# Optimization experiments

Hardware: AMD Instinct MI355X
Metric: run time of the kernel (lower is better)

The kernel has to match this reference:

```python
import jax, jax.numpy as jnp
import numpy as np
from jax import lax

EPS = 1e-12  # torch F.normalize eps


def _unfold3(x):
    # x: [B,C,H,W] -> [B, C*9, H*W]; matches torch F.unfold(k=3, stride=1, pad=1)
    # channel ordering (c, kh, kw), i.e. index = c*9 + kh*3 + kw
    B, C, H, W = x.shape
    xp = jnp.pad(x, ((0, 0), (0, 0), (1, 1), (1, 1)))
    pats = jnp.stack([xp[:, :, i:i + H, j:j + W] for i in range(3) for j in range(3)], axis=2)  # [B,C,9,H,W]
    return pats.reshape(B, C * 9, H * W)


def _fold3(u, H, W):
    # inverse of _unfold3 with overlap-add (torch F.fold, k=3, stride=1, pad=1)
    B, CK, L = u.shape
    C = CK // 9
    u = u.reshape(B, C, 3, 3, H, W)
    canvas = jnp.zeros((B, C, H + 2, W + 2), u.dtype)
    for i in range(3):
        for j in range(3):
            canvas = canvas.at[:, :, i:i + H, j:j + W].add(u[:, :, i, j])
    return canvas[:, :, 1:H + 1, 1:W + 1]


def setup_inputs() -> dict:
    key = jax.random.key(0)
    k1, k2, k3, k4, k5, k6 = jax.random.split(key, 6)
    B, C, H, W = 4, 64, 64, 64
    lr = jax.random.normal(k1, (B, C, H, W), dtype=jnp.float32)
    ref = jax.random.normal(k2, (B, C, H, W), dtype=jnp.float32)
    # fusion: Conv2d(2C, C, 1) then depthwise Conv2d(C, C, 3, groups=C), both with bias
    w1 = jax.random.normal(k3, (C, 2 * C, 1, 1), dtype=jnp.float32) * 0.05
    b1 = jax.random.normal(k4, (C,), dtype=jnp.float32) * 0.05
    wd = jax.random.normal(k5, (C, 1, 3, 3), dtype=jnp.float32) * 0.05
    bd = jax.random.normal(k6, (C,), dtype=jnp.float32) * 0.05
    return {"lr": lr, "ref": ref, "w1": w1, "b1": b1, "wd": wd, "bd": bd}


def reference(lr, ref, w1, b1, wd, bd):
    B, C, H, W = ref.shape
    ref_u = _unfold3(ref)          # [B, 9C, L]
    lr_u = _unfold3(lr)            # [B, 9C, L]
    ref_t = ref_u.transpose(0, 2, 1)  # [B, L, 9C]
    ref_n = ref_t / jnp.maximum(jnp.linalg.norm(ref_t, axis=2, keepdims=True), EPS)
    lr_n = lr_u / jnp.maximum(jnp.linalg.norm(lr_u, axis=1, keepdims=True), EPS)
    R = jnp.einsum('bld,bdm->blm', ref_n, lr_n)  # [B, L, L] cosine correlation
    arg = jnp.argmax(R, axis=1)                  # [B, L] best ref patch per lr position
    T_u = jnp.take_along_axis(ref_u, jnp.broadcast_to(arg[:, None, :], ref_u.shape), axis=2)
    T = _fold3(T_u, H, W)                        # [B, C, H, W]
    x = jnp.concatenate([lr, T], axis=1)         # [B, 2C, H, W]
    dn = ('NCHW', 'OIHW', 'NCHW')
    y = lax.conv_general_dilated(x, w1, (1, 1), 'VALID', dimension_numbers=dn) + b1[None, :, None, None]
    y = lax.conv_general_dilated(y, wd, (1, 1), ((1, 1), (1, 1)), dimension_numbers=dn,
                                 feature_group_count=C) + bd[None, :, None, None]
    return jax.nn.relu(y)
```

## Files before the change

### kernel.cpp

```cpp
#include <hip/hip_runtime.h>
#include <cstdint>
#include <cstddef>


#define BATCH 4
#define CCH 64
#define LPIX 4096
typedef unsigned long long u64;

__device__ __forceinline__ u64 packKey(float v, int idx) {
    unsigned int bits = __float_as_uint(v);
    unsigned int m = (bits & 0x80000000u) ? ~bits : (bits | 0x80000000u);
    return ((u64)m << 32) | (unsigned int)(~(unsigned int)idx);
}

__global__ __launch_bounds__(256) void prep_kernel(const float* __restrict__ ref,
                                                   float* __restrict__ refT,
                                                   float* __restrict__ ssq) {
    __shared__ float s[64 * 65];
    __shared__ float part[256];
    int pt = blockIdx.x, b = blockIdx.y, tid = threadIdx.x;
    const float* rb = ref + ((size_t)b * CCH) * LPIX + pt * 64;
    for (int k = 0; k < 16; ++k) {
        int n = tid + 256 * k;
        int c = n >> 6, p = n & 63;
        s[c * 65 + p] = rb[(size_t)c * LPIX + p];
    }
    __syncthreads();
    {
        int p = tid & 63, g = tid >> 6;
        float acc = 0.f;
        for (int c = g * 16; c < g * 16 + 16; ++c) { float v = s[c * 65 + p]; acc += v * v; }
        part[g * 64 + p] = acc;
    }
    __syncthreads();
    if (tid < 64) {
        float v = part[tid] + part[64 + tid] + part[128 + tid] + part[192 + tid];
        ssq[b * LPIX + pt * 64 + tid] = v;
    }
    float* tb = refT + ((size_t)b * LPIX + pt * 64) * 64;
    for (int k = 0; k < 16; ++k) {
        int n = tid + 256 * k;
        int p = n >> 6, c = n & 63;
        tb[n] = s[c * 65 + p];
    }
}

__global__ __launch_bounds__(256) void invnorm_kernel(const float* __restrict__ ssq,
                                                      float* __restrict__ inv) {
    int t = blockIdx.x * 256 + threadIdx.x;
    int b = t >> 12, p = t & 4095;
    int y = p >> 6, x = p & 63;
    const float* sb = ssq + b * LPIX;
    float n2 = 0.f;
    for (int i = -1; i <= 1; ++i)
        for (int j = -1; j <= 1; ++j) {
            int yy = y + i, xx = x + j;
            if (yy >= 0 && yy < 64 && xx >= 0 && xx < 64) n2 += sb[yy * 64 + xx];
        }
    inv[t] = 1.0f / fmaxf(sqrtf(n2), 1e-12f);
}

__global__ __launch_bounds__(256, 2) void gemmE_kernel(const float* __restrict__ ref,
                                                       const float* __restrict__ lr,
                                                       float* __restrict__ E) {
    __shared__ __align__(16) float As[2 * 4096];
    __shared__ __align__(16) float Bs[2 * 4096];
    int bx = blockIdx.x, by = blockIdx.y, b = blockIdx.z, tid = threadIdx.x;
    const float* Ab = ref + (size_t)b * CCH * LPIX;
    const float* Bb = lr + (size_t)b * CCH * LPIX;
#pragma unroll
    for (int kk = 0; kk < 8; ++kk) {
        int n = tid + 256 * kk;
        int h = n >> 10, c = (n >> 4) & 63, q = n & 15;
        *(float4*)&As[h * 4096 + c * 64 + 4 * q] =
            *(const float4*)&Ab[(size_t)c * LPIX + (2 * by + h) * 64 + 4 * q];
        *(float4*)&Bs[h * 4096 + c * 64 + 4 * q] =
            *(const float4*)&Bb[(size_t)c * LPIX + (2 * bx + h) * 64 + 4 * q];
    }
    __syncthreads();
    int w = tid >> 6, lane = tid & 63, rg = lane >> 3, cg = lane & 7;
    const float* Ap = As + (w >> 1) * 4096 + rg * 8;
    const float* Bp = Bs + (w & 1) * 4096 + cg * 8;
    float acc[8][8] = {};
#pragma unroll 4
    for (int k = 0; k < 64; ++k) {
        float4 a0 = *(const float4*)(Ap + k * 64);
        float4 a1 = *(const float4*)(Ap + k * 64 + 4);
        float4 b0 = *(const float4*)(Bp + k * 64);
        float4 b1 = *(const float4*)(Bp + k * 64 + 4);
        float av[8] = {a0.x, a0.y, a0.z, a0.w, a1.x, a1.y, a1.z, a1.w};
        float bv[8] = {b0.x, b0.y, b0.z, b0.w, b1.x, b1.y, b1.z, b1.w};
#pragma unroll
        for (int i = 0; i < 8; ++i)
#pragma unroll
            for (int j = 0; j < 8; ++j) acc[i][j] = fmaf(av[i], bv[j], acc[i][j]);
    }
    float up[7], lf[7], dn[8], rt[8], um, dpc;
#pragma unroll
    for (int t = 0; t < 7; ++t) up[t] = __shfl(acc[7][t], lane - 8, 64);
    um = __shfl(acc[7][7], lane - 9, 64);
#pragma unroll
    for (int t = 0; t < 7; ++t) lf[t] = __shfl(acc[t][7], lane - 1, 64);
#pragma unroll
    for (int t = 1; t < 8; ++t) dn[t] = __shfl(acc[0][t], lane + 8, 64);
    dpc = __shfl(acc[0][0], lane + 9, 64);
#pragma unroll
    for (int t = 1; t < 8; ++t) rt[t] = __shfl(acc[t][0], lane + 1, 64);

    int r1 = 2 * by + (w >> 1), r2 = 2 * bx + (w & 1);
    float* Et = E + ((size_t)b << 24) + ((size_t)((r1 << 6) + r2) << 12) + (rg * 8) * 64 + cg * 8;
    bool rgt = rg > 0, rlt = rg < 7, cgt = cg > 0, clt = cg < 7;
#pragma unroll
    for (int i = 0; i < 8; ++i) {
        float e[8];
#pragma unroll
        for (int j = 0; j < 8; ++j) {
            float dm, dpv;
            if (i >= 1) dm = (j >= 1) ? acc[i - 1][j - 1] : (cgt ? lf[i - 1] : 0.f);
            else        dm = rgt ? ((j >= 1) ? up[j - 1] : (cgt ? um : 0.f)) : 0.f;
            if (i <= 6) dpv = (j <= 6) ? acc[i + 1][j + 1] : (clt ? rt[i + 1] : 0.f);
            else        dpv = rlt ? ((j <= 6) ? dn[j + 1] : (clt ? dpc : 0.f)) : 0.f;
            e[j] = dm + acc[i][j] + dpv;
        }
        *(float4*)(Et + i * 64)     = make_float4(e[0], e[1], e[2], e[3]);
        *(float4*)(Et + i * 64 + 4) = make_float4(e[4], e[5], e[6], e[7]);
    }
}

__global__ __launch_bounds__(256) void band_kernel(const float* __restrict__ E,
                                                   const float* __restrict__ inv,
                                                   u64* __restrict__ packed) {
    __shared__ u64 red[16 * 65];
    int b = blockIdx.z;
    int k = (int)blockIdx.y - 63;
    int t_lo = k < 0 ? -k : 0;
    int t_hi = 64 - (k > 0 ? k : 0);
    int y0 = t_lo + (int)blockIdx.x * 16;
    if (y0 >= t_hi) return;
    int y1 = y0 + 16 < t_hi ? y0 + 16 : t_hi;
    const float* Ebase = E + ((size_t)b << 24);
    const float* invb = inv + b * LPIX;
    u64* pkb = packed + (size_t)b * LPIX;
    int tid = threadIdx.x;
    int c4 = tid & 15, s = tid >> 4;

    float4 Ea[4], Eb[4], Ec[4];
    auto LOADT = [&](float4* T, int t) {
        if (t >= t_lo && t < t_hi) {
            const float4* tp = (const float4*)(Ebase + ((size_t)(((t + k) << 6) + t) << 12));
#pragma unroll
            for (int i = 0; i < 4; ++i) T[i] = tp[tid + 256 * i];
        } else {
#pragma unroll
            for (int i = 0; i < 4; ++i) T[i] = make_float4(0.f, 0.f, 0.f, 0.f);
        }
    };
    LOADT(Ea, y0 - 1); LOADT(Eb, y0); LOADT(Ec, y0 + 1);

    for (int y = y0; y < y1; ++y) {
        int yprow = (y + k) << 6;
        u64 kc0 = 0, kc1 = 0, kc2 = 0, kc3 = 0;
#pragma unroll
        for (int i = 0; i < 4; ++i) {
            int xr = s + 16 * i;
            float iv = invb[yprow + xr];
            int idx = yprow + xr;
            float vx = (Ea[i].x + Eb[i].x + Ec[i].x) * iv;
            float vy = (Ea[i].y + Eb[i].y + Ec[i].y) * iv;
            float vz = (Ea[i].z + Eb[i].z + Ec[i].z) * iv;
            float vw = (Ea[i].w + Eb[i].w + Ec[i].w) * iv;
            u64 t0 = packKey(vx, idx); kc0 = kc0 > t0 ? kc0 : t0;
            u64 t1 = packKey(vy, idx); kc1 = kc1 > t1 ? kc1 : t1;
            u64 t2 = packKey(vz, idx); kc2 = kc2 > t2 ? kc2 : t2;
            u64 t3 = packKey(vw, idx); kc3 = kc3 > t3 ? kc3 : t3;
        }
        red[s * 65 + 4 * c4 + 0] = kc0;
        red[s * 65 + 4 * c4 + 1] = kc1;
        red[s * 65 + 4 * c4 + 2] = kc2;
        red[s * 65 + 4 * c4 + 3] = kc3;
        __syncthreads();
        if (tid < 64) {
            u64 m = red[tid];
#pragma unroll
            for (int ss = 1; ss < 16; ++ss) {
                u64 v = red[ss * 65 + tid];
                m = m > v ? m : v;
            }
            atomicMax(&pkb[(y << 6) + tid], m);
        }
        __syncthreads();
        if (y + 1 < y1) {
            float4 En[4];
            LOADT(En, y + 2);
#pragma unroll
            for (int i = 0; i < 4; ++i) { Ea[i] = Eb[i]; Eb[i] = Ec[i]; Ec[i] = En[i]; }
        }
    }
}

__global__ __launch_bounds__(256) void gather_kernel(const u64* __restrict__ packed,
                                                     const float* __restrict__ refT,
                                                     float* __restrict__ Tt) {
    int b = blockIdx.y;
    int wave = threadIdx.x >> 6, lane = threadIdx.x & 63;
    int p = blockIdx.x * 4 + wave;
    int py = p >> 6, px = p & 63;
    const u64* pk = packed + (size_t)b * LPIX;
    const float* rT = refT + (size_t)b * LPIX * 64;
    float acc = 0.f;
#pragma unroll
    for (int i = 0; i < 3; ++i)
#pragma unroll
        for (int j = 0; j < 3; ++j) {
            int qy = py + 1 - i, qx = px + 1 - j;
            if ((unsigned)qy >= 64u || (unsigned)qx >= 64u) continue;
            int aidx = (int)(~(unsigned int)pk[qy * 64 + qx]);
            int ry = (aidx >> 6) + i - 1, rx = (aidx & 63) + j - 1;
            if ((unsigned)ry >= 64u || (unsigned)rx >= 64u) continue;
            acc += rT[(size_t)(ry * 64 + rx) * 64 + lane];
        }
    Tt[((size_t)b * LPIX + p) * 64 + lane] = acc;
}

#define XST 36
__global__ __launch_bounds__(256) void conv1_kernel(const float* __restrict__ lr,
                                                    const float* __restrict__ Tt,
                                                    const float* __restrict__ w1,
                                                    const float* __restrict__ b1,
                                                    float* __restrict__ z) {
    __shared__ __align__(16) float xs[128 * XST];
    __shared__ __align__(16) float wsm[64 * 128];
    int pt = blockIdx.x, b = blockIdx.y, tid = threadIdx.x;
    for (int k = 0; k < 8; ++k) {
        int n = tid + 256 * k;
        *(float4*)&wsm[4 * n] = *(const float4*)&w1[4 * n];
    }
    const float* lrb = lr + (size_t)b * CCH * LPIX + pt * 32;
    for (int k = 0; k < 2; ++k) {
        int n = tid + 256 * k;
        int c = n >> 3, q = n & 7;
        *(float4*)&xs[c * XST + 4 * q] = *(const float4*)&lrb[(size_t)c * LPIX + 4 * q];
    }
    const float* Tb = Tt + ((size_t)b * LPIX + pt * 32) * 64;
    for (int k = 0; k < 2; ++k) {
        int n = tid + 256 * k;
        int p = n >> 4, cq = n & 15;
        float4 v = *(const float4*)&Tb[p * 64 + 4 * cq];
        xs[(64 + 4 * cq + 0) * XST + p] = v.x;
        xs[(64 + 4 * cq + 1) * XST + p] = v.y;
        xs[(64 + 4 * cq + 2) * XST + p] = v.z;
        xs[(64 + 4 * cq + 3) * XST + p] = v.w;
    }
    __syncthreads();
    int p = tid & 31, g = tid >> 5;
    float acc[8];
#pragma unroll
    for (int t = 0; t < 8; ++t) acc[t] = b1[g * 8 + t];
    for (int c = 0; c < 128; ++c) {
        float xv = xs[c * XST + p];
#pragma unroll
        for (int t = 0; t < 8; ++t) acc[t] = fmaf(wsm[(g * 8 + t) * 128 + c], xv, acc[t]);
    }
    float* zb = z + (size_t)b * CCH * LPIX + pt * 32;
#pragma unroll
    for (int t = 0; t < 8; ++t) zb[(size_t)(g * 8 + t) * LPIX + p] = acc[t];
}

__global__ __launch_bounds__(256) void dw_kernel(const float* __restrict__ z,
                                                 const float* __restrict__ wd,
                                                 const float* __restrict__ bd,
                                                 float* __restrict__ out) {
    __shared__ __align__(16) float zs[4096];
    int c = blockIdx.x, b = blockIdx.y, tid = threadIdx.x;
    const float* zb = z + ((size_t)b * CCH + c) * LPIX;
    for (int k = 0; k < 4; ++k) {
        int n = tid + 256 * k;
        *(float4*)&zs[4 * n] = *(const float4*)&zb[4 * n];
    }
    __syncthreads();
    float w[9];
#pragma unroll
    for (int t = 0; t < 9; ++t) w[t] = wd[c * 9 + t];
    float bias = bd[c];
    float* ob = out + ((size_t)b * CCH + c) * LPIX;
    for (int s = 0; s < 16; ++s) {
        int p = tid + 256 * s;
        int y = p >> 6, x = p & 63;
        float acc = bias;
#pragma unroll
        for (int i = 0; i < 3; ++i) {
            int yy = y + i - 1;
            if ((unsigned)yy >= 64u) continue;
#pragma unroll
            for (int j = 0; j < 3; ++j) {
                int xx = x + j - 1;
                if ((unsigned)xx >= 64u) continue;
                acc = fmaf(zs[yy * 64 + xx], w[i * 3 + j], acc);
            }
        }
        ob[p] = fmaxf(acc, 0.f);
    }
}

extern "C" void kernel_launch(void* const* d_in, const int* in_sizes, int n_in,
                              void* d_out, int out_size, void* d_ws, size_t ws_size,
                              hipStream_t stream) {
    const float* lr  = (const float*)d_in[0];
    const float* ref = (const float*)d_in[1];
    const float* w1  = (const float*)d_in[2];
    const float* b1  = (const float*)d_in[3];
    const float* wd  = (const float*)d_in[4];
    const float* bd  = (const float*)d_in[5];
    float* out = (float*)d_out;

    float* ws = (float*)d_ws;
    float* refT = ws;
    float* ssq  = refT + (size_t)1048576;
    float* inv  = ssq + 16384;
    u64* packed = (u64*)(inv + 16384);
    float* Tt = (float*)(packed + 16384);
    float* z  = Tt + (size_t)1048576;
    float* E  = z + (size_t)1048576;

    int full = (ws_size >= (size_t)12845056 + 4ull * 67108864ull) ? 1 : 0;

    hipMemsetAsync(packed, 0, (size_t)BATCH * LPIX * sizeof(u64), stream);
    prep_kernel<<<dim3(64, BATCH), 256, 0, stream>>>(ref, refT, ssq);
    invnorm_kernel<<<dim3(64), 256, 0, stream>>>(ssq, inv);
    if (full) {
        gemmE_kernel<<<dim3(32, 32, BATCH), 256, 0, stream>>>(ref, lr, E);
        band_kernel<<<dim3(4, 127, BATCH), 256, 0, stream>>>(E, inv, packed);
    } else {
        for (int b = 0; b < BATCH; ++b) {
            gemmE_kernel<<<dim3(32, 32, 1), 256, 0, stream>>>(
                ref + (size_t)b * CCH * LPIX, lr + (size_t)b * CCH * LPIX, E);
            band_kernel<<<dim3(4, 127, 1), 256, 0, stream>>>(
                E, inv + (size_t)b * LPIX, packed + (size_t)b * LPIX);
        }
    }
    gather_kernel<<<dim3(1024, BATCH), 256, 0, stream>>>(packed, refT, Tt);
    conv1_kernel<<<dim3(128, BATCH), 256, 0, stream>>>(lr, Tt, w1, b1, z);
    dw_kernel<<<dim3(64, BATCH), 256, 0, stream>>>(z, wd, bd, out);
}
```

Before: 302.7 us.

## Fuse correlation GEMM with banded argmax to avoid materialising E

Replaces the separate GEMM-writing-E kernel and banded reduction kernel with a single diagonal-walking kernel that computes each 64x64 patch-correlation tile, applies the 3x3 diagonal stencil and the row-direction 3-tap sum in registers, and does the normalized argmax inline with wave shuffles and atomicMax. This removes the large intermediate E buffer write and read. In exchange each block is a single wave with high register pressure (P, Q, acc arrays), loads tiles without overlap, and processes diagonal segments serially.

New measurement: 452.1 us. +49.4%, slower.

```diff
diff --git a/kernel.cpp b/kernel.cpp
--- a/kernel.cpp
+++ b/kernel.cpp
@@ -6,6 +6,7 @@
 #define BATCH 4
 #define CCH 64
 #define LPIX 4096
+#define SEG 8
 typedef unsigned long long u64;
 
 __device__ __forceinline__ u64 packKey(float v, int idx) {
@@ -61,140 +62,137 @@
     inv[t] = 1.0f / fmaxf(sqrtf(n2), 1e-12f);
 }
 
-__global__ __launch_bounds__(256, 2) void gemmE_kernel(const float* __restrict__ ref,
-                                                       const float* __restrict__ lr,
-                                                       float* __restrict__ E) {
-    __shared__ __align__(16) float As[2 * 4096];
-    __shared__ __align__(16) float Bs[2 * 4096];
-    int bx = blockIdx.x, by = blockIdx.y, b = blockIdx.z, tid = threadIdx.x;
-    const float* Ab = ref + (size_t)b * CCH * LPIX;
-    const float* Bb = lr + (size_t)b * CCH * LPIX;
-#pragma unroll
-    for (int kk = 0; kk < 8; ++kk) {
-        int n = tid + 256 * kk;
-        int h = n >> 10, c = (n >> 4) & 63, q = n & 15;
-        *(float4*)&As[h * 4096 + c * 64 + 4 * q] =
-            *(const float4*)&Ab[(size_t)c * LPIX + (2 * by + h) * 64 + 4 * q];
-        *(float4*)&Bs[h * 4096 + c * 64 + 4 * q] =
-            *(const float4*)&Bb[(size_t)c * LPIX + (2 * bx + h) * 64 + 4 * q];
-    }
-    __syncthreads();
-    int w = tid >> 6, lane = tid & 63, rg = lane >> 3, cg = lane & 7;
-    const float* Ap = As + (w >> 1) * 4096 + rg * 8;
-    const float* Bp = Bs + (w & 1) * 4096 + cg * 8;
-    float acc[8][8] = {};
-#pragma unroll 4
-    for (int k = 0; k < 64; ++k) {
-        float4 a0 = *(const float4*)(Ap + k * 64);
-        float4 a1 = *(const float4*)(Ap + k * 64 + 4);
-        float4 b0 = *(const float4*)(Bp + k * 64);
-        float4 b1 = *(const float4*)(Bp + k * 64 + 4);
-        float av[8] = {a0.x, a0.y, a0.z, a0.w, a1.x, a1.y, a1.z, a1.w};
-        float bv[8] = {b0.x, b0.y, b0.z, b0.w, b1.x, b1.y, b1.z, b1.w};
-#pragma unroll
-        for (int i = 0; i < 8; ++i)
-#pragma unroll
-            for (int j = 0; j < 8; ++j) acc[i][j] = fmaf(av[i], bv[j], acc[i][j]);
-    }
-    float up[7], lf[7], dn[8], rt[8], um, dpc;
-#pragma unroll
-    for (int t = 0; t < 7; ++t) up[t] = __shfl(acc[7][t], lane - 8, 64);
-    um = __shfl(acc[7][7], lane - 9, 64);
-#pragma unroll
-    for (int t = 0; t < 7; ++t) lf[t] = __shfl(acc[t][7], lane - 1, 64);
-#pragma unroll
-    for (int t = 1; t < 8; ++t) dn[t] = __shfl(acc[0][t], lane + 8, 64);
-    dpc = __shfl(acc[0][0], lane + 9, 64);
-#pragma unroll
-    for (int t = 1; t < 8; ++t) rt[t] = __shfl(acc[t][0], lane + 1, 64);
-
-    int r1 = 2 * by + (w >> 1), r2 = 2 * bx + (w & 1);
-    float* Et = E + ((size_t)b << 24) + ((size_t)((r1 << 6) + r2) << 12) + (rg * 8) * 64 + cg * 8;
-    bool rgt = rg > 0, rlt = rg < 7, cgt = cg > 0, clt = cg < 7;
-#pragma unroll
-    for (int i = 0; i < 8; ++i) {
-        float e[8];
-#pragma unroll
-        for (int j = 0; j < 8; ++j) {
-            float dm, dpv;
-            if (i >= 1) dm = (j >= 1) ? acc[i - 1][j - 1] : (cgt ? lf[i - 1] : 0.f);
-            else        dm = rgt ? ((j >= 1) ? up[j - 1] : (cgt ? um : 0.f)) : 0.f;
-            if (i <= 6) dpv = (j <= 6) ? acc[i + 1][j + 1] : (clt ? rt[i + 1] : 0.f);
-            else        dpv = rlt ? ((j <= 6) ? dn[j + 1] : (clt ? dpc : 0.f)) : 0.f;
-            e[j] = dm + acc[i][j] + dpv;
-        }
-        *(float4*)(Et + i * 64)     = make_float4(e[0], e[1], e[2], e[3]);
-        *(float4*)(Et + i * 64 + 4) = make_float4(e[4], e[5], e[6], e[7]);
-    }
-}
-
-__global__ __launch_bounds__(256) void band_kernel(const float* __restrict__ E,
-                                                   const float* __restrict__ inv,
-                                                   u64* __restrict__ packed) {
-    __shared__ u64 red[16 * 65];
+__global__ __launch_bounds__(64) void diag_kernel(const float* __restrict__ ref,
+                                                  const float* __restrict__ lr,
+                                                  const float* __restrict__ inv,
+                                                  u64* __restrict__ packed) {
+    __shared__ __align__(16) float As[32 * 64];
+    __shared__ __align__(16) float Bs[32 * 64];
+    int k = (int)blockIdx.x - 63;
     int b = blockIdx.z;
-    int k = (int)blockIdx.y - 63;
     int t_lo = k < 0 ? -k : 0;
     int t_hi = 64 - (k > 0 ? k : 0);
-    int y0 = t_lo + (int)blockIdx.x * 16;
-    if (y0 >= t_hi) return;
-    int y1 = y0 + 16 < t_hi ? y0 + 16 : t_hi;
-    const float* Ebase = E + ((size_t)b << 24);
+    int t0i = t_lo + (int)blockIdx.y * SEG;
+    if (t0i >= t_hi) return;
+    int t1i = t0i + SEG < t_hi ? t0i + SEG : t_hi;
+
+    const float* refb = ref + (size_t)b * CCH * LPIX;
+    const float* lrb  = lr  + (size_t)b * CCH * LPIX;
     const float* invb = inv + b * LPIX;
     u64* pkb = packed + (size_t)b * LPIX;
-    int tid = threadIdx.x;
-    int c4 = tid & 15, s = tid >> 4;
-
-    float4 Ea[4], Eb[4], Ec[4];
-    auto LOADT = [&](float4* T, int t) {
-        if (t >= t_lo && t < t_hi) {
-            const float4* tp = (const float4*)(Ebase + ((size_t)(((t + k) << 6) + t) << 12));
-#pragma unroll
-            for (int i = 0; i < 4; ++i) T[i] = tp[tid + 256 * i];
+
+    int lane = threadIdx.x;
+    int rg = lane >> 3, cg = lane & 7;
+    bool rgt = rg > 0, rlt = rg < 7, cgt = cg > 0, clt = cg < 7;
+
+    float P[8][8] = {}, Q[8][8] = {};
+
+    for (int t = t0i - 1; t <= t1i; ++t) {
+        bool tv = (t >= t_lo) && (t < t_hi);
+        bool fin = (t - 1 >= t0i) && (t - 1 < t1i);
+        int yprow = (t - 1 + k) << 6;
+        float iv[8], bv[8];
+        int bi[8];
+        if (fin) {
+            float4 iv0 = *(const float4*)&invb[yprow + rg * 8];
+            float4 iv1 = *(const float4*)&invb[yprow + rg * 8 + 4];
+            iv[0] = iv0.x; iv[1] = iv0.y; iv[2] = iv0.z; iv[3] = iv0.w;
+            iv[4] = iv1.x; iv[5] = iv1.y; iv[6] = iv1.z; iv[7] = iv1.w;
+#pragma unroll
+            for (int j = 0; j < 8; ++j) { bv[j] = -3.4e38f; bi[j] = 0; }
+        }
+        if (tv) {
+            int r1 = t + k, r2 = t;
+            float acc[8][8] = {};
+#pragma unroll
+            for (int h = 0; h < 2; ++h) {
+                const float* Ag = refb + (size_t)(h * 32) * LPIX + r1 * 64;
+                const float* Bg = lrb  + (size_t)(h * 32) * LPIX + r2 * 64;
+                __syncthreads();
+#pragma unroll
+                for (int it = 0; it < 8; ++it) {
+                    int n = it * 64 + lane;
+                    int c = n >> 4, q = n & 15;
+                    *(float4*)&As[c * 64 + 4 * q] = *(const float4*)&Ag[(size_t)c * LPIX + 4 * q];
+                    *(float4*)&Bs[c * 64 + 4 * q] = *(const float4*)&Bg[(size_t)c * LPIX + 4 * q];
+                }
+                __syncthreads();
+                const float* Ap = As + rg * 8;
+                const float* Bp = Bs + cg * 8;
+#pragma unroll 4
+                for (int kk = 0; kk < 32; ++kk) {
+                    float4 a0 = *(const float4*)(Ap + kk * 64);
+                    float4 a1 = *(const float4*)(Ap + kk * 64 + 4);
+                    float4 b0 = *(const float4*)(Bp + kk * 64);
+                    float4 b1 = *(const float4*)(Bp + kk * 64 + 4);
+                    float av[8] = {a0.x, a0.y, a0.z, a0.w, a1.x, a1.y, a1.z, a1.w};
+                    float bw[8] = {b0.x, b0.y, b0.z, b0.w, b1.x, b1.y, b1.z, b1.w};
+#pragma unroll
+                    for (int i = 0; i < 8; ++i)
+#pragma unroll
+                        for (int j = 0; j < 8; ++j) acc[i][j] = fmaf(av[i], bw[j], acc[i][j]);
+                }
+            }
+            float up[7], lf[7], dn[8], rt[8], um, dpc;
+#pragma unroll
+            for (int q = 0; q < 7; ++q) up[q] = __shfl(acc[7][q], lane - 8, 64);
+            um = __shfl(acc[7][7], lane - 9, 64);
+#pragma unroll
+            for (int q = 0; q < 7; ++q) lf[q] = __shfl(acc[q][7], lane - 1, 64);
+#pragma unroll
+            for (int q = 1; q < 8; ++q) dn[q] = __shfl(acc[0][q], lane + 8, 64);
+            dpc = __shfl(acc[0][0], lane + 9, 64);
+#pragma unroll
+            for (int q = 1; q < 8; ++q) rt[q] = __shfl(acc[q][0], lane + 1, 64);
+#pragma unroll
+            for (int i = 0; i < 8; ++i) {
+#pragma unroll
+                for (int j = 0; j < 8; ++j) {
+                    float dm, dpv;
+                    if (i >= 1) dm = (j >= 1) ? acc[i - 1][j - 1] : (cgt ? lf[i - 1] : 0.f);
+                    else        dm = rgt ? ((j >= 1) ? up[j - 1] : (cgt ? um : 0.f)) : 0.f;
+                    if (i <= 6) dpv = (j <= 6) ? acc[i + 1][j + 1] : (clt ? rt[i + 1] : 0.f);
+                    else        dpv = rlt ? ((j <= 6) ? dn[j + 1] : (clt ? dpc : 0.f)) : 0.f;
+                    float e = dm + acc[i][j] + dpv;
+                    float sv = P[i][j] + e;
+                    P[i][j] = Q[i][j] + e;
+                    Q[i][j] = e;
+                    if (fin) {
+                        float v = sv * iv[i];
+                        if (v > bv[j]) { bv[j] = v; bi[j] = i; }
+                    }
+                }
+            }
         } else {
 #pragma unroll
-            for (int i = 0; i < 4; ++i) T[i] = make_float4(0.f, 0.f, 0.f, 0.f);
-        }
-    };
-    LOADT(Ea, y0 - 1); LOADT(Eb, y0); LOADT(Ec, y0 + 1);
-
-    for (int y = y0; y < y1; ++y) {
-        int yprow = (y + k) << 6;
-        u64 kc0 = 0, kc1 = 0, kc2 = 0, kc3 = 0;
-#pragma unroll
-        for (int i = 0; i < 4; ++i) {
-            int xr = s + 16 * i;
-            float iv = invb[yprow + xr];
-            int idx = yprow + xr;
-            float vx = (Ea[i].x + Eb[i].x + Ec[i].x) * iv;
-            float vy = (Ea[i].y + Eb[i].y + Ec[i].y) * iv;
-            float vz = (Ea[i].z + Eb[i].z + Ec[i].z) * iv;
-            float vw = (Ea[i].w + Eb[i].w + Ec[i].w) * iv;
-            u64 t0 = packKey(vx, idx); kc0 = kc0 > t0 ? kc0 : t0;
-            u64 t1 = packKey(vy, idx); kc1 = kc1 > t1 ? kc1 : t1;
-            u64 t2 = packKey(vz, idx); kc2 = kc2 > t2 ? kc2 : t2;
-            u64 t3 = packKey(vw, idx); kc3 = kc3 > t3 ? kc3 : t3;
-        }
-        red[s * 65 + 4 * c4 + 0] = kc0;
-        red[s * 65 + 4 * c4 + 1] = kc1;
-        red[s * 65 + 4 * c4 + 2] = kc2;
-        red[s * 65 + 4 * c4 + 3] = kc3;
-        __syncthreads();
-        if (tid < 64) {
-            u64 m = red[tid];
-#pragma unroll
-            for (int ss = 1; ss < 16; ++ss) {
-                u64 v = red[ss * 65 + tid];
-                m = m > v ? m : v;
+            for (int i = 0; i < 8; ++i)
+#pragma unroll
+                for (int j = 0; j < 8; ++j) {
+                    float sv = P[i][j];
+                    P[i][j] = Q[i][j];
+                    Q[i][j] = 0.f;
+                    if (fin) {
+                        float v = sv * iv[i];
+                        if (v > bv[j]) { bv[j] = v; bi[j] = i; }
+                    }
+                }
+        }
+        if (fin) {
+            u64 key[8];
+#pragma unroll
+            for (int j = 0; j < 8; ++j) key[j] = packKey(bv[j], yprow + rg * 8 + bi[j]);
+#pragma unroll
+            for (int d = 8; d <= 32; d <<= 1)
+#pragma unroll
+                for (int j = 0; j < 8; ++j) {
+                    u64 o = __shfl_xor(key[j], d, 64);
+                    key[j] = key[j] > o ? key[j] : o;
+                }
+            if (rg == 0) {
+                int cb = ((t - 1) << 6) + cg * 8;
+#pragma unroll
+                for (int j = 0; j < 8; ++j) atomicMax(&pkb[cb + j], key[j]);
             }
-            atomicMax(&pkb[(y << 6) + tid], m);
-        }
-        __syncthreads();
-        if (y + 1 < y1) {
-            float4 En[4];
-            LOADT(En, y + 2);
-#pragma unroll
-            for (int i = 0; i < 4; ++i) { Ea[i] = Eb[i]; Eb[i] = Ec[i]; Ec[i] = En[i]; }
         }
     }
 }
@@ -321,24 +319,11 @@
     u64* packed = (u64*)(inv + 16384);
     float* Tt = (float*)(packed + 16384);
     float* z  = Tt + (size_t)1048576;
-    float* E  = z + (size_t)1048576;
-
-    int full = (ws_size >= (size_t)12845056 + 4ull * 67108864ull) ? 1 : 0;
 
     hipMemsetAsync(packed, 0, (size_t)BATCH * LPIX * sizeof(u64), stream);
     prep_kernel<<<dim3(64, BATCH), 256, 0, stream>>>(ref, refT, ssq);
     invnorm_kernel<<<dim3(64), 256, 0, stream>>>(ssq, inv);
-    if (full) {
-        gemmE_kernel<<<dim3(32, 32, BATCH), 256, 0, stream>>>(ref, lr, E);
-        band_kernel<<<dim3(4, 127, BATCH), 256, 0, stream>>>(E, inv, packed);
-    } else {
-        for (int b = 0; b < BATCH; ++b) {
-            gemmE_kernel<<<dim3(32, 32, 1), 256, 0, stream>>>(
-                ref + (size_t)b * CCH * LPIX, lr + (size_t)b * CCH * LPIX, E);
-            band_kernel<<<dim3(4, 127, 1), 256, 0, stream>>>(
-                E, inv + (size_t)b * LPIX, packed + (size_t)b * LPIX);
-        }
-    }
+    diag_kernel<<<dim3(127, 8, BATCH), 64, 0, stream>>>(ref, lr, inv, packed);
     gather_kernel<<<dim3(1024, BATCH), 256, 0, stream>>>(packed, refT, Tt);
     conv1_kernel<<<dim3(128, BATCH), 256, 0, stream>>>(lr, Tt, w1, b1, z);
     dw_kernel<<<dim3(64, BATCH), 256, 0, stream>>>(z, wd, bd, out);
```
